# Kernel optimization log

Measured on AMD Instinct MI355X. Metric: run time of the kernel, lower is better.

The kernel has to match this reference:

```python
import jax, jax.numpy as jnp
import numpy as np

N, K, D = 16384, 200, 64  # n_samples, n_components, n_features (8x8 patches)
LOG_2PI = np.float32(np.log(2.0 * np.pi))


def setup_inputs() -> dict:
    rng = np.random.default_rng(0)
    # Build SPD covariances and derive precisions_cholesky exactly like the module:
    # cov_chol = cholesky(cov, lower); prec_chol = solve(cov_chol, I).T
    A = rng.normal(size=(K, D, D))
    cov = A @ A.transpose(0, 2, 1) + D * np.eye(D)  # well-conditioned SPD
    cov_chol = np.linalg.cholesky(cov)  # lower triangular [K,D,D]
    eye = np.broadcast_to(np.eye(D), (K, D, D))
    prec_chol = np.linalg.solve(cov_chol, eye).transpose(0, 2, 1).astype(np.float32)
    means = rng.normal(size=(K, D)).astype(np.float32)
    key = jax.random.key(0)
    x = jax.random.normal(key, (N, D), dtype=jnp.float32)
    return {"x": x, "means": jnp.asarray(means), "prec_chol": jnp.asarray(prec_chol)}


def reference(x, means, prec_chol):
    """Batched GMM log-prob (fused version of estimate_log_prob_torch).

    log_prob[n,k] = -0.5*(D*log(2pi) + ||x_n L_k - mu_k L_k||^2) + log|det L_k|
    where L_k = precisions_cholesky[k].
    """
    n_features = x.shape[1]
    # y[n,k,e] = x @ L_k  -- one batched GEMM instead of K small matmuls
    y = jnp.einsum('nd,kde->nke', x, prec_chol)
    mu_prec = jnp.einsum('kd,kde->ke', means, prec_chol)  # mu_k @ L_k, [K,D]
    log_prob = jnp.sum(jnp.square(y - mu_prec[None, :, :]), axis=-1)  # [N,K]
    # log det of cholesky of precision = sum of log of diagonal entries
    log_det = jnp.sum(jnp.log(jnp.diagonal(prec_chol, axis1=1, axis2=2)), axis=1)  # [K]
    return -0.5 * (n_features * LOG_2PI + log_prob) + log_det[None, :]
```

## Files before the change

kernel.cpp:

```cpp
#include <hip/hip_runtime.h>
#include <hip/hip_bf16.h>
#include <stdint.h>

typedef __bf16 bf16x4v __attribute__((ext_vector_type(4)));
typedef __bf16 bf16x8  __attribute__((ext_vector_type(8)));
typedef float  f32x4   __attribute__((ext_vector_type(4)));
typedef float  f32x2   __attribute__((ext_vector_type(2)));
typedef float  f32x16  __attribute__((ext_vector_type(16)));

#define KC 200
#define KB 8
#define CBASE (-58.8120661251f)


__global__ __launch_bounds__(256) void prep(const float* __restrict__ prec,
                                            const float* __restrict__ means,
                                            const float* __restrict__ x,
                                            __bf16* __restrict__ Ltf,
                                            float* __restrict__ muL,
                                            float* __restrict__ ckh,
                                            __bf16* __restrict__ xb) {
    const int tid = threadIdx.x;
    if (blockIdx.x >= 400) {
        const size_t base = (size_t)(blockIdx.x - 400) * 4096;
        #pragma unroll
        for (int r = 0; r < 4; ++r) {
            size_t idx = base + r * 1024 + tid * 4;
            float4 v = *(const float4*)(x + idx);
            bf16x4v o = {(__bf16)v.x, (__bf16)v.y, (__bf16)v.z, (__bf16)v.w};
            *(bf16x4v*)(xb + idx) = o;
        }
        return;
    }
    __shared__ float sP[64][40];
    __shared__ float sM[64];
    const int k = blockIdx.x >> 1, h = blockIdx.x & 1;
    const float* pk = prec + (size_t)k * 4096 + h * 32;
    #pragma unroll
    for (int it = 0; it < 2; ++it) {
        int f4 = tid + it * 256;
        int d = f4 >> 3, c = (f4 & 7) * 4;
        float4 v = *(const float4*)(pk + (size_t)d * 64 + c);
        *(float4*)&sP[d][c] = v;
    }
    if (tid < 16) *(float4*)&sM[tid * 4] = ((const float4*)(means + (size_t)k * 64))[tid];
    __syncthreads();
    {
        int lane = tid & 63, ki = tid >> 6;
        int hp = lane >> 5, l31 = lane & 31;
        bf16x8 o;
        #pragma unroll
        for (int j = 0; j < 8; ++j) o[j] = (__bf16)sP[16 * ki + 8 * hp + j][l31];
        *(bf16x8*)(Ltf + (size_t)k * 4096 + (h * 4 + ki) * 512 + lane * 8) = o;
    }
    if (tid < 32) {
        int e = tid;
        float m = 0.f;
        #pragma unroll 8
        for (int d = 0; d < 64; ++d) m = fmaf(sM[d], sP[d][e], m);
        muL[k * 64 + h * 32 + e] = m;
        float l = __logf(sP[h * 32 + e][e]);
        #pragma unroll
        for (int mm = 16; mm >= 1; mm >>= 1) l += __shfl_xor(l, mm, 64);
        if (e == 0) ckh[h * KC + k] = l;
    }
}

#define GLL16(gp_, lp_) \
    __builtin_amdgcn_global_load_lds((__attribute__((address_space(1))) const void*)(gp_), \
                                     (__attribute__((address_space(3))) void*)(lp_), 16, 0, 0)

__global__ __launch_bounds__(256, 4) void gmm_main(const __bf16* __restrict__ xb,
                                                   const __bf16* __restrict__ Ltf,
                                                   const float* __restrict__ muL,
                                                   const float* __restrict__ ckh,
                                                   float* __restrict__ out) {
    __shared__ __align__(16) __bf16 sX[256 * 64];
    __shared__ __align__(16) float  sOutT[KB][256];

    const int tid  = threadIdx.x;
    const int wave = tid >> 6, lane = tid & 63;
    const int hp   = lane >> 5;
    const int l31  = lane & 31;
    const int r8   = lane >> 3, s8 = lane & 7;
    const int row0 = blockIdx.x * 256;
    const int k0   = blockIdx.y * KB;
    char* sXc = (char*)sX;

    #pragma unroll
    for (int i = 0; i < 8; ++i) {
        int t = wave * 8 + i;
        GLL16(xb + (size_t)(row0 + t * 8 + r8) * 64 + (s8 ^ r8) * 8, sXc + t * 1024);
    }
    __syncthreads();

    #pragma unroll
    for (int ks = 0; ks < 2; ++ks) {
        const int k  = k0 + wave * 2 + ks;
        const int kl = wave * 2 + ks;
        bf16x8 lf[2][4];
        #pragma unroll
        for (int et = 0; et < 2; ++et)
            #pragma unroll
            for (int ki = 0; ki < 4; ++ki)
                lf[et][ki] = *(const bf16x8*)(Ltf + (size_t)k * 4096 + (et * 4 + ki) * 512 + lane * 8);
        f32x16 c0[2];
        #pragma unroll
        for (int et = 0; et < 2; ++et)
            #pragma unroll
            for (int q2 = 0; q2 < 4; ++q2) {
                f32x4 m = *(const f32x4*)(muL + (size_t)k * 64 + et * 32 + 8 * q2 + 4 * hp);
                c0[et][4 * q2 + 0] = -m[0]; c0[et][4 * q2 + 1] = -m[1];
                c0[et][4 * q2 + 2] = -m[2]; c0[et][4 * q2 + 3] = -m[3];
            }
        const float ck = ckh[k] + ckh[KC + k] + CBASE;

        #pragma unroll
        for (int rt = 0; rt < 8; ++rt) {
            bf16x8 xf[4];
            #pragma unroll
            for (int ki = 0; ki < 4; ++ki)
                xf[ki] = *(const bf16x8*)(sXc + (rt * 32 + l31) * 128
                                          + (((2 * ki + hp) ^ (l31 & 7)) << 4));
            f32x16 a0 = __builtin_amdgcn_mfma_f32_32x32x16_bf16(lf[0][0], xf[0], c0[0], 0, 0, 0);
            f32x16 a1 = __builtin_amdgcn_mfma_f32_32x32x16_bf16(lf[1][0], xf[0], c0[1], 0, 0, 0);
            #pragma unroll
            for (int ki = 1; ki < 4; ++ki) {
                a0 = __builtin_amdgcn_mfma_f32_32x32x16_bf16(lf[0][ki], xf[ki], a0, 0, 0, 0);
                a1 = __builtin_amdgcn_mfma_f32_32x32x16_bf16(lf[1][ki], xf[ki], a1, 0, 0, 0);
            }
            f32x2 p2 = {0.f, 0.f};
            #pragma unroll
            for (int i = 0; i < 8; ++i) {
                f32x2 u = {a0[2 * i], a0[2 * i + 1]};
                f32x2 v = {a1[2 * i], a1[2 * i + 1]};
                p2 += u * u;
                p2 += v * v;
            }
            float pr = p2[0] + p2[1];
            pr += __shfl_xor(pr, 32, 64);
            if (hp == 0) sOutT[kl][rt * 32 + l31] = fmaf(-0.5f, pr, ck);
        }
    }
    __syncthreads();

    {
        float vals[KB];
        #pragma unroll
        for (int kk = 0; kk < KB; ++kk) vals[kk] = sOutT[kk][tid];
        f32x4 a = {vals[0], vals[1], vals[2], vals[3]};
        f32x4 b = {vals[4], vals[5], vals[6], vals[7]};
        float* op = out + (size_t)(row0 + tid) * KC + k0;
        *(f32x4*)op = a;
        *(f32x4*)(op + 4) = b;
    }
}

extern "C" void kernel_launch(void* const* d_in, const int* in_sizes, int n_in,
                              void* d_out, int out_size, void* d_ws, size_t ws_size,
                              hipStream_t stream) {
    const float* x     = (const float*)d_in[0];
    const float* means = (const float*)d_in[1];
    const float* prec  = (const float*)d_in[2];
    float* out = (float*)d_out;

    __bf16* Ltf = (__bf16*)d_ws;
    float*  muL = (float*)((char*)d_ws + 1638400);
    float*  ckh = (float*)((char*)d_ws + 1689600);
    __bf16* xb  = (__bf16*)((char*)d_ws + 1691200);

    prep<<<656, 256, 0, stream>>>(prec, means, x, Ltf, muL, ckh, xb);
    gmm_main<<<dim3(64, KC / KB), 256, 0, stream>>>(xb, Ltf, muL, ckh, out);
}
```

Before: 93.90 us.

## Halve row tile to 128 and prefetch first component's weights before barrier

The main kernel now covers 128 rows per block instead of 256, which doubles the grid to 128x25 blocks and halves the LDS footprint. That should raise occupancy and give more blocks to spread across CUs. The first component's L, mu and constant are loaded into registers before the barrier so those loads overlap the x tile transfer. The cost is that the L fragments are re-read from global memory twice as often across the grid. The output store is reshaped so each thread writes one 16-byte vector.

After: 93.65 us. About the same (-0.3%).

```diff
diff --git a/kernel.cpp b/kernel.cpp
--- a/kernel.cpp
+++ b/kernel.cpp
@@ -75,48 +75,67 @@
                                                    const float* __restrict__ muL,
                                                    const float* __restrict__ ckh,
                                                    float* __restrict__ out) {
-    __shared__ __align__(16) __bf16 sX[256 * 64];
-    __shared__ __align__(16) float  sOutT[KB][256];
+    __shared__ __align__(16) __bf16 sX[128 * 64];
+    __shared__ __align__(16) float  sOutT[KB][128];
 
     const int tid  = threadIdx.x;
     const int wave = tid >> 6, lane = tid & 63;
     const int hp   = lane >> 5;
     const int l31  = lane & 31;
     const int r8   = lane >> 3, s8 = lane & 7;
-    const int row0 = blockIdx.x * 256;
+    const int row0 = blockIdx.x * 128;
     const int k0   = blockIdx.y * KB;
     char* sXc = (char*)sX;
 
     #pragma unroll
-    for (int i = 0; i < 8; ++i) {
-        int t = wave * 8 + i;
+    for (int i = 0; i < 4; ++i) {
+        int t = wave * 4 + i;
         GLL16(xb + (size_t)(row0 + t * 8 + r8) * 64 + (s8 ^ r8) * 8, sXc + t * 1024);
     }
+
+    const int kA = k0 + wave * 2;
+    bf16x8 lf[2][4];
+    #pragma unroll
+    for (int et = 0; et < 2; ++et)
+        #pragma unroll
+        for (int ki = 0; ki < 4; ++ki)
+            lf[et][ki] = *(const bf16x8*)(Ltf + (size_t)kA * 4096 + (et * 4 + ki) * 512 + lane * 8);
+    f32x16 c0[2];
+    #pragma unroll
+    for (int et = 0; et < 2; ++et)
+        #pragma unroll
+        for (int q2 = 0; q2 < 4; ++q2) {
+            f32x4 m = *(const f32x4*)(muL + (size_t)kA * 64 + et * 32 + 8 * q2 + 4 * hp);
+            c0[et][4 * q2 + 0] = -m[0]; c0[et][4 * q2 + 1] = -m[1];
+            c0[et][4 * q2 + 2] = -m[2]; c0[et][4 * q2 + 3] = -m[3];
+        }
+    float ck = ckh[kA] + ckh[KC + kA] + CBASE;
+
     __syncthreads();
 
     #pragma unroll
     for (int ks = 0; ks < 2; ++ks) {
-        const int k  = k0 + wave * 2 + ks;
         const int kl = wave * 2 + ks;
-        bf16x8 lf[2][4];
-        #pragma unroll
-        for (int et = 0; et < 2; ++et)
+        if (ks == 1) {
+            const int kB_ = k0 + wave * 2 + 1;
             #pragma unroll
-            for (int ki = 0; ki < 4; ++ki)
-                lf[et][ki] = *(const bf16x8*)(Ltf + (size_t)k * 4096 + (et * 4 + ki) * 512 + lane * 8);
-        f32x16 c0[2];
-        #pragma unroll
-        for (int et = 0; et < 2; ++et)
+            for (int et = 0; et < 2; ++et)
+                #pragma unroll
+                for (int ki = 0; ki < 4; ++ki)
+                    lf[et][ki] = *(const bf16x8*)(Ltf + (size_t)kB_ * 4096 + (et * 4 + ki) * 512 + lane * 8);
             #pragma unroll
-            for (int q2 = 0; q2 < 4; ++q2) {
-                f32x4 m = *(const f32x4*)(muL + (size_t)k * 64 + et * 32 + 8 * q2 + 4 * hp);
-                c0[et][4 * q2 + 0] = -m[0]; c0[et][4 * q2 + 1] = -m[1];
-                c0[et][4 * q2 + 2] = -m[2]; c0[et][4 * q2 + 3] = -m[3];
-            }
-        const float ck = ckh[k] + ckh[KC + k] + CBASE;
+            for (int et = 0; et < 2; ++et)
+                #pragma unroll
+                for (int q2 = 0; q2 < 4; ++q2) {
+                    f32x4 m = *(const f32x4*)(muL + (size_t)kB_ * 64 + et * 32 + 8 * q2 + 4 * hp);
+                    c0[et][4 * q2 + 0] = -m[0]; c0[et][4 * q2 + 1] = -m[1];
+                    c0[et][4 * q2 + 2] = -m[2]; c0[et][4 * q2 + 3] = -m[3];
+                }
+            ck = ckh[kB_] + ckh[KC + kB_] + CBASE;
+        }
 
         #pragma unroll
-        for (int rt = 0; rt < 8; ++rt) {
+        for (int rt = 0; rt < 4; ++rt) {
             bf16x8 xf[4];
             #pragma unroll
             for (int ki = 0; ki < 4; ++ki)
@@ -145,14 +164,11 @@
     __syncthreads();
 
     {
-        float vals[KB];
+        const int r = tid >> 1, h = tid & 1;
+        f32x4 a;
         #pragma unroll
-        for (int kk = 0; kk < KB; ++kk) vals[kk] = sOutT[kk][tid];
-        f32x4 a = {vals[0], vals[1], vals[2], vals[3]};
-        f32x4 b = {vals[4], vals[5], vals[6], vals[7]};
-        float* op = out + (size_t)(row0 + tid) * KC + k0;
-        *(f32x4*)op = a;
-        *(f32x4*)(op + 4) = b;
+        for (int j = 0; j < 4; ++j) a[j] = sOutT[h * 4 + j][r];
+        *(f32x4*)(out + (size_t)(row0 + r) * KC + k0 + h * 4) = a;
     }
 }
 
@@ -170,5 +186,5 @@
     __bf16* xb  = (__bf16*)((char*)d_ws + 1691200);
 
     prep<<<656, 256, 0, stream>>>(prec, means, x, Ltf, muL, ckh, xb);
-    gmm_main<<<dim3(64, KC / KB), 256, 0, stream>>>(xb, Ltf, muL, ckh, out);
+    gmm_main<<<dim3(128, KC / KB), 256, 0, stream>>>(xb, Ltf, muL, ckh, out);
 }
```
